# Performance work log

Measured on AMD Instinct MI355X. Metric: run time of the kernel, lower is better.

## Reference

```python
import jax, jax.numpy as jnp
import numpy as np

EPS = 1e-5
CURVE_LEN = 16


def gather_neighbors(feature, idx):
    # feature: [B, C, N], idx: [B, N, k] -> [B, C, N, k]
    return jax.vmap(lambda f, i: f[:, i])(feature, idx)


def cloud_walk(feature, knn_idx):
    # feature: [B, C, N], knn_idx: [B, N, k] -> walk_index [B, N, 16] (int)
    B, C, N = feature.shape
    neigh = gather_neighbors(feature, knn_idx)                 # [B, C, N, k]
    sim = jnp.einsum('bcn,bcnk->bnk', feature, neigh)          # [B, N, k]
    attn = jax.nn.softmax(sim, axis=-1)
    top4 = jax.lax.top_k(attn, 4)[1]                           # [B, N, 4]
    tmp = top4.reshape(B * N, 4)
    nxt = top4[:, :, 1]                                        # [B, N]
    walks = [nxt]
    for _ in range(CURVE_LEN - 1):
        # faithful to original: index rows of tmp by previous step's values
        nxt = tmp[nxt.reshape(-1), 1].reshape(B, N)
        walks.append(nxt)
    return jnp.stack(walks, axis=-1)                           # [B, N, 16]


def self_attention_layer(feature, walk_idx, Wq, bq, Wk, bk, Wv, bv, gamma, beta):
    # feature: [B, C, N], walk_idx: [B, N, 16]
    wf = gather_neighbors(feature, walk_idx)                   # [B, C, N, 16]
    wf = jnp.transpose(wf, (0, 2, 3, 1))                       # [B, N, 16, C]
    center = jnp.transpose(feature, (0, 2, 1))[:, :, None, :]  # [B, N, 1, C]
    win = jnp.concatenate([wf, center], axis=2)                # [B, N, 17, C]
    Q = win @ Wq.T + bq
    K = win @ Wk.T + bk
    V = win @ Wv.T + bv
    sim = jnp.einsum('bnic,bnjc->bnij', Q, K)                  # [B, N, 17, 17]
    attn = jax.nn.softmax(sim, axis=-1)
    # original einsum 'bnkk,bnkc->bnc' => diagonal of attention weights V
    d = jnp.diagonal(attn, axis1=2, axis2=3)                   # [B, N, 17]
    out = jnp.einsum('bnk,bnkc->bnc', d, V)                    # [B, N, C]
    x = jnp.transpose(out, (0, 2, 1))                          # [B, C, N]
    # BatchNorm1d, training mode: stats over (batch, points), biased variance
    mean = jnp.mean(x, axis=(0, 2), keepdims=True)
    var = jnp.mean((x - mean) ** 2, axis=(0, 2), keepdims=True)
    x = gamma[None, :, None] * (x - mean) / jnp.sqrt(var + EPS) + beta[None, :, None]
    x = jax.nn.relu(x)
    return feature + x


def setup_inputs() -> dict:
    key = jax.random.key(0)
    B, C, N, k = 2, 64, 32768, 16
    ks = jax.random.split(key, 10)
    feature = jax.random.normal(ks[0], (B, C, N), dtype=jnp.float32)
    knn_idx = jax.random.randint(ks[1], (B, N, k), 0, N)
    Wq = jax.random.normal(ks[2], (3, C, C), dtype=jnp.float32) * 0.05
    bq = jax.random.normal(ks[3], (3, C), dtype=jnp.float32) * 0.05
    Wk = jax.random.normal(ks[4], (3, C, C), dtype=jnp.float32) * 0.05
    bk = jax.random.normal(ks[5], (3, C), dtype=jnp.float32) * 0.05
    Wv = jax.random.normal(ks[6], (3, C, C), dtype=jnp.float32) * 0.05
    bv = jax.random.normal(ks[7], (3, C), dtype=jnp.float32) * 0.05
    gamma = jnp.ones((3, C), dtype=jnp.float32)
    beta = jnp.zeros((3, C), dtype=jnp.float32)
    return {"feature": feature, "knn_idx": knn_idx, "Wq": Wq, "bq": bq,
            "Wk": Wk, "bk": bk, "Wv": Wv, "bv": bv, "gamma": gamma, "beta": beta}


def reference(feature, knn_idx, Wq, bq, Wk, bk, Wv, bv, gamma, beta):
    walk_idx = cloud_walk(feature, knn_idx)
    heads = []
    f = feature
    for i in range(3):
        f = self_attention_layer(f, walk_idx, Wq[i], bq[i], Wk[i], bk[i],
                                 Wv[i], bv[i], gamma[i], beta[i])
        heads.append(f)
    return jnp.concatenate(heads, axis=1)  # [B, 3C, N]
```

## Files before the change

### kernel.cpp

```cpp
#include <hip/hip_runtime.h>
#include <math.h>

#define NB 2
#define NC 64
#define NN 32768
#define NPTS (NB*NN)
#define NWAVES 1056
#define NSLOTS 67584

typedef _Float16 half_t;
typedef _Float16 f16x8 __attribute__((ext_vector_type(8)));
typedef _Float16 f16x4 __attribute__((ext_vector_type(4)));
typedef float f32x4 __attribute__((ext_vector_type(4)));

__global__ void k_transpose(const float* __restrict__ f, float* __restrict__ fT,
                            half_t* __restrict__ xh) {
    int blk = blockIdx.x;
    int b = blk / (NN/64);
    int n0 = (blk % (NN/64)) * 64;
    __shared__ float tile[64][65];
    int t = threadIdx.x;
    int dn = t & 63, c0 = t >> 6;
    for (int i = 0; i < 16; ++i) {
        int c = c0 + i*4;
        tile[c][dn] = f[((size_t)(b*NC + c))*NN + n0 + dn];
    }
    __syncthreads();
    int o = t & 63, d0 = t >> 6;
    for (int i = 0; i < 16; ++i) {
        int dn2 = d0 + i*4;
        size_t idx = ((size_t)(b*NN + n0 + dn2))*64 + o;
        float v = tile[o][dn2];
        fT[idx] = v;
        xh[idx] = (half_t)v;
    }
}

__global__ __launch_bounds__(256, 4) void k_s2(const float* __restrict__ fT,
                                               const int* __restrict__ knn,
                                               int* __restrict__ s2buf) {
    int t = threadIdx.x;
    int gp = blockIdx.x * 32 + (t >> 3);
    int l8 = t & 7;
    int q4 = l8 & 3;
    int h  = l8 >> 2;
    int b = gp >> 15;
    const float4* cen4 = (const float4*)(fT + (size_t)gp*64 + q4*16);
    float4 c0 = cen4[0], c1 = cen4[1], c2 = cen4[2], c3 = cen4[3];
    float own[8];
    #pragma unroll
    for (int kk = 0; kk < 8; ++kk) {
        int idx = knn[(gp << 4) + h*8 + kk];
        const float4* nb = (const float4*)(fT + ((size_t)(b*NN + idx))*64 + q4*16);
        float4 n0 = nb[0], n1 = nb[1], n2 = nb[2], n3 = nb[3];
        double a = 0.0;
        a += (double)c0.x*(double)n0.x + (double)c0.y*(double)n0.y
           + (double)c0.z*(double)n0.z + (double)c0.w*(double)n0.w;
        a += (double)c1.x*(double)n1.x + (double)c1.y*(double)n1.y
           + (double)c1.z*(double)n1.z + (double)c1.w*(double)n1.w;
        a += (double)c2.x*(double)n2.x + (double)c2.y*(double)n2.y
           + (double)c2.z*(double)n2.z + (double)c2.w*(double)n2.w;
        a += (double)c3.x*(double)n3.x + (double)c3.y*(double)n3.y
           + (double)c3.z*(double)n3.z + (double)c3.w*(double)n3.w;
        a += __shfl_xor(a, 1, 64);
        a += __shfl_xor(a, 2, 64);
        own[kk] = (float)a;
    }
    float sims[16];
    #pragma unroll
    for (int kk = 0; kk < 8; ++kk) {
        float oth = __shfl_xor(own[kk], 4, 64);
        sims[kk]     = h ? oth : own[kk];
        sims[kk + 8] = h ? own[kk] : oth;
    }
    float m = sims[0];
    #pragma unroll
    for (int k = 1; k < 16; ++k) m = fmaxf(m, sims[k]);
    float e[16]; float Z = 0.f;
    #pragma unroll
    for (int k = 0; k < 16; ++k) { e[k] = expf(sims[k]-m); Z += e[k]; }
    float b1 = -1.f, b2 = -1.f; int i1 = -1, i2 = -1;
    #pragma unroll
    for (int k = 0; k < 16; ++k) {
        float a = e[k]/Z;
        if (a > b1)      { b2 = b1; i2 = i1; b1 = a; i1 = k; }
        else if (a > b2) { b2 = a; i2 = k; }
    }
    if (l8 == 0) s2buf[gp] = i2;
}

__global__ void k_walk(const int* __restrict__ s2buf, int* __restrict__ walkrows) {
    __shared__ int T[16];
    int t = threadIdx.x;
    if (t < 16) T[t] = s2buf[t];
    __syncthreads();
    if (t < 16) {
        int w = t;
        walkrows[t*16 + 0] = w;
        for (int s = 1; s < 16; ++s) { w = T[w]; walkrows[t*16 + s] = w; }
    }
}

__global__ void k_init(int* __restrict__ slotlist, int* __restrict__ wavebucket) {
    int idx = blockIdx.x*256 + threadIdx.x;
    if (idx < NSLOTS) slotlist[idx] = -1;
    if (idx < NWAVES) wavebucket[idx] = -1;
}

__global__ void k_hist2(const int* __restrict__ s2buf, int* __restrict__ bh) {
    __shared__ int hst[32];
    int t = threadIdx.x, blk = blockIdx.x;
    if (t < 32) hst[t] = 0;
    __syncthreads();
    int p = blk*256 + t;
    int bucket = (p >> 15)*16 + s2buf[p];
    atomicAdd(&hst[bucket], 1);
    __syncthreads();
    if (t < 32) bh[t*256 + blk] = hst[t];
}

__global__ void k_prefix(const int* __restrict__ bh, int* __restrict__ blockoff,
                         int* __restrict__ wavebucket) {
    __shared__ int tot[32], wst[32];
    int t = threadIdx.x;
    if (t < 32) {
        int s = 0;
        for (int b = 0; b < 256; ++b) s += bh[t*256 + b];
        tot[t] = s;
    }
    __syncthreads();
    if (t == 0) {
        int off = 0;
        for (int i = 0; i < 32; ++i) {
            wst[i] = off;
            off += ((tot[i] + 63) >> 6) << 6;
        }
    }
    __syncthreads();
    if (t < 32) {
        int run = wst[t];
        for (int b = 0; b < 256; ++b) {
            blockoff[t*256 + b] = run;
            run += bh[t*256 + b];
        }
        int w0 = wst[t] >> 6, nw = (tot[t] + 63) >> 6;
        for (int w = 0; w < nw; ++w) wavebucket[w0 + w] = t;
    }
}

__global__ void k_scatter2(const int* __restrict__ s2buf,
                           const int* __restrict__ blockoff,
                           int* __restrict__ slotlist) {
    __shared__ int hst[32], base[32];
    int t = threadIdx.x, blk = blockIdx.x;
    if (t < 32) { hst[t] = 0; base[t] = blockoff[t*256 + blk]; }
    __syncthreads();
    int p = blk*256 + t;
    int bucket = (p >> 15)*16 + s2buf[p];
    int r = atomicAdd(&hst[bucket], 1);
    slotlist[base[bucket] + r] = p;
}

__global__ __launch_bounds__(256) void k_precomp(
        const float* __restrict__ fT,
        const float* __restrict__ Wq, const float* __restrict__ bq,
        const float* __restrict__ Wk, const float* __restrict__ bk,
        const float* __restrict__ Wv, const float* __restrict__ bv,
        const int* __restrict__ walkrows,
        half_t* __restrict__ Pq16, half_t* __restrict__ Pk16,
        half_t* __restrict__ PvT16, float* __restrict__ Pstat,
        half_t* __restrict__ wh) {
    int blk = blockIdx.x;
    int b = blk >> 4, sv = blk & 15;
    size_t bsv16 = (size_t)(b*16 + sv) * 1024;
    int bs48 = (b*16 + sv)*48;
    __shared__ float win[16][64];
    __shared__ float Wl[64][65];
    __shared__ float qw[16][65], kw[16][65];
    __shared__ float simw[16][17];
    __shared__ int wr[16];
    int t = threadIdx.x;
    #pragma unroll
    for (int j = 0; j < 2; ++j) {
        int idx = j*8192 + blk*256 + t;
        if (idx < 12288) {
            float v = idx < 4096 ? Wq[idx] : (idx < 8192 ? Wk[idx-4096] : Wv[idx-8192]);
            wh[idx] = (half_t)v;
        }
    }
    if (t < 16) wr[t] = walkrows[sv*16 + t];
    __syncthreads();
    #pragma unroll
    for (int i = 0; i < 4; ++i) {
        int idx = t + i*256; int tt = idx >> 6, c = idx & 63;
        win[tt][c] = fT[((size_t)(b*NN + wr[tt]))*64 + c];
    }
    int wv = t >> 6, lane = t & 63;
    for (int m = 0; m < 3; ++m) {
        const float* W  = m == 0 ? Wq : (m == 1 ? Wk : Wv);
        const float* bb = m == 0 ? bq : (m == 1 ? bk : bv);
        __syncthreads();
        #pragma unroll
        for (int i = 0; i < 16; ++i) {
            int idx = t + i*256;
            Wl[idx >> 6][idx & 63] = W[idx];
        }
        __syncthreads();
        float acc[4] = {0.f, 0.f, 0.f, 0.f};
        for (int c = 0; c < 64; ++c) {
            float w_ = Wl[lane][c];
            #pragma unroll
            for (int r = 0; r < 4; ++r) acc[r] = fmaf(w_, win[wv*4 + r][c], acc[r]);
        }
        float bias = bb[lane];
        #pragma unroll
        for (int r = 0; r < 4; ++r) {
            int tt = wv*4 + r;
            float val = acc[r] + bias;
            if (m == 0)      { qw[tt][lane] = val; Pq16[bsv16 + tt*64 + lane] = (half_t)val; }
            else if (m == 1) { kw[tt][lane] = val; Pk16[bsv16 + tt*64 + lane] = (half_t)val; }
            else             {                     PvT16[bsv16 + lane*16 + tt] = (half_t)val; }
        }
    }
    __syncthreads();
    {
        int i = t >> 4, j = t & 15;
        float acc = 0.f;
        for (int o = 0; o < 64; ++o) acc = fmaf(qw[i][o], kw[j][o], acc);
        simw[i][j] = acc;
    }
    __syncthreads();
    if (t < 16) {
        float mx = simw[t][0];
        for (int j = 1; j < 16; ++j) mx = fmaxf(mx, simw[t][j]);
        float z = 0.f;
        for (int j = 0; j < 16; ++j) z += expf(simw[t][j] - mx);
        Pstat[bs48 + t*3 + 0] = mx;
        Pstat[bs48 + t*3 + 1] = z;
        Pstat[bs48 + t*3 + 2] = simw[t][t];
    }
}

__global__ __launch_bounds__(256) void k_gemm(
        const half_t* __restrict__ xh, const int* __restrict__ slotlist, int s0,
        const half_t* __restrict__ wh,
        const float* __restrict__ bq, const float* __restrict__ bk,
        const float* __restrict__ bv,
        half_t* __restrict__ qh, half_t* __restrict__ kh, half_t* __restrict__ vh) {
    __shared__ __align__(16) half_t XO[256*72];
    __shared__ __align__(16) half_t WL[192*72];
    int t = threadIdx.x;
    int lane = t & 63, wv = t >> 6;
    size_t go = (size_t)blockIdx.x * 256 * 64;
    {
        int srow = slotlist[s0 + blockIdx.x*256 + t];
        int prow = srow < 0 ? 0 : srow;
        const uint4* src = (const uint4*)(xh + (size_t)prow*64);
        #pragma unroll
        for (int j = 0; j < 8; ++j) *(uint4*)&XO[t*72 + j*8] = src[j];
    }
    #pragma unroll
    for (int j = 0; j < 6; ++j) {
        int idx8 = t + j*256;
        int row = idx8 >> 3, c0 = (idx8 & 7) * 8;
        *(uint4*)&WL[row*72 + c0] = *(const uint4*)(wh + idx8*8);
    }
    __syncthreads();
    int m15 = lane & 15, k0 = (lane >> 4) * 8;
    int ar = wv*64 + m15;
    f16x8 a00 = *(const f16x8*)&XO[(ar    )*72 + k0];
    f16x8 a01 = *(const f16x8*)&XO[(ar    )*72 + k0 + 32];
    f16x8 a10 = *(const f16x8*)&XO[(ar+16)*72 + k0];
    f16x8 a11 = *(const f16x8*)&XO[(ar+16)*72 + k0 + 32];
    f16x8 a20 = *(const f16x8*)&XO[(ar+32)*72 + k0];
    f16x8 a21 = *(const f16x8*)&XO[(ar+32)*72 + k0 + 32];
    f16x8 a30 = *(const f16x8*)&XO[(ar+48)*72 + k0];
    f16x8 a31 = *(const f16x8*)&XO[(ar+48)*72 + k0 + 32];
    __syncthreads();
    #pragma unroll 1
    for (int m = 0; m < 3; ++m) {
        const float* bias = m == 0 ? bq : (m == 1 ? bk : bv);
        half_t* outp      = m == 0 ? qh : (m == 1 ? kh : vh);
        int wb = m*64 + m15;
        f16x8 b00 = *(const f16x8*)&WL[(wb    )*72 + k0];
        f16x8 b01 = *(const f16x8*)&WL[(wb    )*72 + k0 + 32];
        f16x8 b10 = *(const f16x8*)&WL[(wb+16)*72 + k0];
        f16x8 b11 = *(const f16x8*)&WL[(wb+16)*72 + k0 + 32];
        f16x8 b20 = *(const f16x8*)&WL[(wb+32)*72 + k0];
        f16x8 b21 = *(const f16x8*)&WL[(wb+32)*72 + k0 + 32];
        f16x8 b30 = *(const f16x8*)&WL[(wb+48)*72 + k0];
        f16x8 b31 = *(const f16x8*)&WL[(wb+48)*72 + k0 + 32];
        float bs0 = bias[m15], bs1 = bias[16+m15], bs2 = bias[32+m15], bs3 = bias[48+m15];
        f32x4 Z = {0.f, 0.f, 0.f, 0.f};
        f32x4 c00=Z,c01=Z,c02=Z,c03=Z, c10=Z,c11=Z,c12=Z,c13=Z;
        f32x4 c20=Z,c21=Z,c22=Z,c23=Z, c30=Z,c31=Z,c32=Z,c33=Z;
        #define MM(i,j) \
            c##i##j = __builtin_amdgcn_mfma_f32_16x16x32_f16(a##i##0, b##j##0, c##i##j, 0,0,0); \
            c##i##j = __builtin_amdgcn_mfma_f32_16x16x32_f16(a##i##1, b##j##1, c##i##j, 0,0,0);
        MM(0,0) MM(0,1) MM(0,2) MM(0,3)
        MM(1,0) MM(1,1) MM(1,2) MM(1,3)
        MM(2,0) MM(2,1) MM(2,2) MM(2,3)
        MM(3,0) MM(3,1) MM(3,2) MM(3,3)
        #undef MM
        __syncthreads();
        int r0 = wv*64 + ((lane >> 4) << 2);
        #define WR(i,j,bsj) { \
            XO[(r0 + i*16 + 0)*64 + j*16 + m15] = (half_t)(c##i##j[0] + bsj); \
            XO[(r0 + i*16 + 1)*64 + j*16 + m15] = (half_t)(c##i##j[1] + bsj); \
            XO[(r0 + i*16 + 2)*64 + j*16 + m15] = (half_t)(c##i##j[2] + bsj); \
            XO[(r0 + i*16 + 3)*64 + j*16 + m15] = (half_t)(c##i##j[3] + bsj); }
        WR(0,0,bs0) WR(0,1,bs1) WR(0,2,bs2) WR(0,3,bs3)
        WR(1,0,bs0) WR(1,1,bs1) WR(1,2,bs2) WR(1,3,bs3)
        WR(2,0,bs0) WR(2,1,bs1) WR(2,2,bs2) WR(2,3,bs3)
        WR(3,0,bs0) WR(3,1,bs1) WR(3,2,bs2) WR(3,3,bs3)
        #undef WR
        __syncthreads();
        #pragma unroll
        for (int j = 0; j < 8; ++j) {
            int idx = (j*256 + t) * 8;
            *(uint4*)(outp + go + idx) = *(const uint4*)&XO[idx];
        }
    }
}

__global__ __launch_bounds__(256) void k_comb4(
        const half_t* __restrict__ qh, const half_t* __restrict__ kh,
        const half_t* __restrict__ vh,
        const half_t* __restrict__ Pq16, const half_t* __restrict__ Pk16,
        const half_t* __restrict__ PvT16, const float* __restrict__ Pstat,
        const int* __restrict__ slotlist, const int* __restrict__ wavebucket,
        half_t* __restrict__ xo, int s0) {
    int t = threadIdx.x, j = t >> 6, lane = t & 63;
    int wslot = blockIdx.x*64;
    int gbase = s0 + wslot;
    int bucket = wavebucket[gbase >> 6];
    if (bucket < 0) return;
    int m15 = lane & 15, g4 = lane >> 4;
    int k0h = g4 * 8;
    size_t bsv16 = (size_t)bucket << 10;
    int bs48 = bucket * 48;

    f16x8 pqA0 = *(const f16x8*)&Pq16[bsv16 + m15*64 + k0h];
    f16x8 pqA1 = *(const f16x8*)&Pq16[bsv16 + m15*64 + k0h + 32];
    f16x8 pkA0 = *(const f16x8*)&Pk16[bsv16 + m15*64 + k0h];
    f16x8 pkA1 = *(const f16x8*)&Pk16[bsv16 + m15*64 + k0h + 32];
    f16x4 pvB0 = *(const f16x4*)&PvT16[bsv16 + (0*16 + m15)*16 + g4*4];
    f16x4 pvB1 = *(const f16x4*)&PvT16[bsv16 + (1*16 + m15)*16 + g4*4];
    f16x4 pvB2 = *(const f16x4*)&PvT16[bsv16 + (2*16 + m15)*16 + g4*4];
    f16x4 pvB3 = *(const f16x4*)&PvT16[bsv16 + (3*16 + m15)*16 + g4*4];
    float pm[4], pz[4], dg[4];
    #pragma unroll
    for (int r = 0; r < 4; ++r) {
        pm[r] = Pstat[bs48 + (g4*4+r)*3 + 0];
        pz[r] = Pstat[bs48 + (g4*4+r)*3 + 1];
        dg[r] = Pstat[bs48 + (g4*4+r)*3 + 2];
    }
    int4 pid4 = *(const int4*)&slotlist[gbase + j*16 + g4*4];

    const half_t* kp = kh + (size_t)(wslot + j*16 + m15)*64;
    const half_t* qp = qh + (size_t)(wslot + j*16 + m15)*64;
    f16x8 kB0 = *(const f16x8*)&kp[k0h];
    f16x8 kB1 = *(const f16x8*)&kp[k0h + 32];
    f16x8 qB0 = *(const f16x8*)&qp[k0h];
    f16x8 qB1 = *(const f16x8*)&qp[k0h + 32];
    f32x4 Zz = {0.f,0.f,0.f,0.f};
    f32x4 sp = __builtin_amdgcn_mfma_f32_16x16x32_f16(pqA0, kB0, Zz, 0,0,0);
    sp = __builtin_amdgcn_mfma_f32_16x16x32_f16(pqA1, kB1, sp, 0,0,0);
    f32x4 tp = __builtin_amdgcn_mfma_f32_16x16x32_f16(pkA0, qB0, Zz, 0,0,0);
    tp = __builtin_amdgcn_mfma_f32_16x16x32_f16(pkA1, qB1, tp, 0,0,0);
    float up = 0.f;
    #pragma unroll
    for (int e = 0; e < 8; ++e) {
        up = fmaf((float)qB0[e], (float)kB0[e], up);
        up = fmaf((float)qB1[e], (float)kB1[e], up);
    }
    up += __shfl_xor(up, 16, 64);
    up += __shfl_xor(up, 32, 64);
    float d0, d1, d2, d3;
    {
        float mi, zi;
        mi = fmaxf(pm[0], sp[0]); zi = pz[0]*expf(pm[0]-mi) + expf(sp[0]-mi); d0 = expf(dg[0]-mi)/zi;
        mi = fmaxf(pm[1], sp[1]); zi = pz[1]*expf(pm[1]-mi) + expf(sp[1]-mi); d1 = expf(dg[1]-mi)/zi;
        mi = fmaxf(pm[2], sp[2]); zi = pz[2]*expf(pm[2]-mi) + expf(sp[2]-mi); d2 = expf(dg[2]-mi)/zi;
        mi = fmaxf(pm[3], sp[3]); zi = pz[3]*expf(pm[3]-mi) + expf(sp[3]-mi); d3 = expf(dg[3]-mi)/zi;
    }
    float tmax = fmaxf(fmaxf(tp[0], tp[1]), fmaxf(tp[2], tp[3]));
    tmax = fmaxf(tmax, __shfl_xor(tmax, 16, 64));
    tmax = fmaxf(tmax, __shfl_xor(tmax, 32, 64));
    float mc = fmaxf(tmax, up);
    float ze = expf(tp[0]-mc) + expf(tp[1]-mc) + expf(tp[2]-mc) + expf(tp[3]-mc);
    ze += __shfl_xor(ze, 16, 64);
    ze += __shfl_xor(ze, 32, 64);
    float ec = expf(up - mc);
    float dcen = ec / (ze + ec);
    f16x4 dA; dA[0] = (half_t)d0; dA[1] = (half_t)d1; dA[2] = (half_t)d2; dA[3] = (half_t)d3;

    float dc0 = __shfl(dcen, g4*4 + 0, 64);
    float dc1 = __shfl(dcen, g4*4 + 1, 64);
    float dc2 = __shfl(dcen, g4*4 + 2, 64);
    float dc3 = __shfl(dcen, g4*4 + 3, 64);
    int p0 = pid4.x, p1 = pid4.y, p2 = pid4.z, p3 = pid4.w;
    size_t vb0 = (size_t)(wslot + j*16 + g4*4 + 0)*64;
    size_t vb1 = (size_t)(wslot + j*16 + g4*4 + 1)*64;
    size_t vb2 = (size_t)(wslot + j*16 + g4*4 + 2)*64;
    size_t vb3 = (size_t)(wslot + j*16 + g4*4 + 3)*64;
    #pragma unroll
    for (int jc = 0; jc < 4; ++jc) {
        f16x4 pvB = jc == 0 ? pvB0 : (jc == 1 ? pvB1 : (jc == 2 ? pvB2 : pvB3));
        f32x4 Z2 = {0.f,0.f,0.f,0.f};
        f32x4 acc = __builtin_amdgcn_mfma_f32_16x16x16f16(dA, pvB, Z2, 0,0,0);
        int c = jc*16 + m15;
        float v0 = (float)vh[vb0 + c];
        float v1 = (float)vh[vb1 + c];
        float v2 = (float)vh[vb2 + c];
        float v3 = (float)vh[vb3 + c];
        if (p0 >= 0) xo[(size_t)p0*64 + c] = (half_t)(acc[0] + dc0*v0);
        if (p1 >= 0) xo[(size_t)p1*64 + c] = (half_t)(acc[1] + dc1*v1);
        if (p2 >= 0) xo[(size_t)p2*64 + c] = (half_t)(acc[2] + dc2*v2);
        if (p3 >= 0) xo[(size_t)p3*64 + c] = (half_t)(acc[3] + dc3*v3);
    }
}

__global__ __launch_bounds__(256) void k_reduce(const half_t* __restrict__ x,
                                                float* __restrict__ part) {
    __shared__ float ls[4][64], lq[4][64];
    int t = threadIdx.x, q = t >> 6, c = t & 63;
    size_t base = ((size_t)blockIdx.x*128 + q*32) * 64;
    float s = 0.f, sq = 0.f;
    for (int r = 0; r < 32; ++r) {
        float v = (float)x[base + r*64 + c];
        s += v; sq = fmaf(v, v, sq);
    }
    ls[q][c] = s; lq[q][c] = sq;
    __syncthreads();
    if (q == 0) {
        float S = ls[0][c] + ls[1][c] + ls[2][c] + ls[3][c];
        float Q = lq[0][c] + lq[1][c] + lq[2][c] + lq[3][c];
        part[blockIdx.x*64 + c] = S;
        part[512*64 + blockIdx.x*64 + c] = Q;
    }
}

__global__ __launch_bounds__(256) void k_stats(const float* __restrict__ part,
                                               float* __restrict__ mv) {
    __shared__ float ls[4][64], lq[4][64];
    int t = threadIdx.x, q = t >> 6, c = t & 63;
    float s = 0.f, sq = 0.f;
    for (int r = q*128; r < q*128 + 128; ++r) {
        s  += part[r*64 + c];
        sq += part[512*64 + r*64 + c];
    }
    ls[q][c] = s; lq[q][c] = sq;
    __syncthreads();
    if (q == 0) {
        float S = ls[0][c] + ls[1][c] + ls[2][c] + ls[3][c];
        float Q = lq[0][c] + lq[1][c] + lq[2][c] + lq[3][c];
        float mean = S / (float)NPTS;
        float var  = Q / (float)NPTS - mean*mean;
        mv[c] = mean; mv[64 + c] = var;
    }
}

__global__ void k_norm(const half_t* __restrict__ x, float* __restrict__ fT,
                       const float* __restrict__ mv,
                       const float* __restrict__ gamma, const float* __restrict__ beta,
                       float* __restrict__ out, int l, half_t* __restrict__ xh) {
    int blk = blockIdx.x;
    int b = blk / (NN/64);
    int n0 = (blk % (NN/64)) * 64;
    __shared__ float tile[64][65];
    int t = threadIdx.x;
    int c = t & 63, d0 = t >> 6;
    float mean = mv[c], var = mv[64+c];
    float inv = 1.0f / sqrtf(var + 1e-5f);
    float ga = gamma[c], be = beta[c];
    for (int i = 0; i < 16; ++i) {
        int dn = d0 + i*4;
        size_t pi = ((size_t)(b*NN + n0 + dn))*64 + c;
        float xv = (float)x[pi];
        float y = fT[pi] + fmaxf(ga * (xv - mean) * inv + be, 0.f);
        fT[pi] = y;
        xh[pi] = (half_t)y;
        tile[dn][c] = y;
    }
    __syncthreads();
    int dn2 = t & 63, c0 = t >> 6;
    for (int i = 0; i < 16; ++i) {
        int cc = c0 + i*4;
        out[((size_t)(b*192 + l*64 + cc))*NN + n0 + dn2] = tile[dn2][cc];
    }
}

extern "C" void kernel_launch(void* const* d_in, const int* in_sizes, int n_in,
                              void* d_out, int out_size, void* d_ws, size_t ws_size,
                              hipStream_t stream) {
    const float* feature = (const float*)d_in[0];
    const int*   knn     = (const int*)d_in[1];
    const float* Wq = (const float*)d_in[2];
    const float* bq = (const float*)d_in[3];
    const float* Wk = (const float*)d_in[4];
    const float* bk = (const float*)d_in[5];
    const float* Wv = (const float*)d_in[6];
    const float* bv = (const float*)d_in[7];
    const float* gamma = (const float*)d_in[8];
    const float* beta  = (const float*)d_in[9];
    float* out = (float*)d_out;

    char* ws = (char*)d_ws;
    float*  fT    = (float*) ws;
    half_t* xh    = (half_t*)(ws + 16777216);
    half_t* xo    = (half_t*)(ws + 25165824);
    int*    s2buf = (int*)   (ws + 33554432);
    int*    walkrows = (int*)(ws + 33816576);
    half_t* Pq16  = (half_t*)(ws + 33817600);
    half_t* Pk16  = (half_t*)(ws + 33883136);
    half_t* PvT16 = (half_t*)(ws + 33948672);
    float*  Pstat = (float*) (ws + 34014208);
    float*  part  = (float*) (ws + 34020352);
    float*  mv    = (float*) (ws + 34282496);
    half_t* wh    = (half_t*)(ws + 34283008);
    int*    bh        = (int*)(ws + 34307584);
    int*    blockoff  = (int*)(ws + 34340352);
    int*    wavebucket= (int*)(ws + 34373120);
    int*    slotlist  = (int*)(ws + 34377344);
    size_t  qkv_off = 34647680;

    size_t avail = ws_size > qkv_off ? ws_size - qkv_off : 0;
    size_t chunk = avail / 384;
    chunk = (chunk / 256) * 256;
    if (chunk > (size_t)NSLOTS) chunk = NSLOTS;
    if (chunk < 256) chunk = 256;
    half_t* qh = (half_t*)(ws + qkv_off);
    half_t* kh = qh + chunk*64;
    half_t* vh = kh + chunk*64;

    k_transpose<<<NB*(NN/64), 256, 0, stream>>>(feature, fT, xh);
    k_s2<<<NPTS/32, 256, 0, stream>>>(fT, knn, s2buf);
    k_walk<<<1, 64, 0, stream>>>(s2buf, walkrows);
    k_init<<<NSLOTS/256, 256, 0, stream>>>(slotlist, wavebucket);
    k_hist2<<<NPTS/256, 256, 0, stream>>>(s2buf, bh);
    k_prefix<<<1, 256, 0, stream>>>(bh, blockoff, wavebucket);
    k_scatter2<<<NPTS/256, 256, 0, stream>>>(s2buf, blockoff, slotlist);

    for (int l = 0; l < 3; ++l) {
        k_precomp<<<32, 256, 0, stream>>>(fT, Wq + l*4096, bq + l*64,
                                          Wk + l*4096, bk + l*64,
                                          Wv + l*4096, bv + l*64,
                                          walkrows, Pq16, Pk16, PvT16, Pstat, wh);
        for (size_t s0 = 0; s0 < NSLOTS; s0 += chunk) {
            size_t cn = (s0 + chunk <= NSLOTS) ? chunk : (NSLOTS - s0);
            k_gemm<<<(unsigned)(cn/256), 256, 0, stream>>>(xh, slotlist, (int)s0, wh,
                                                           bq + l*64, bk + l*64, bv + l*64,
                                                           qh, kh, vh);
            k_comb4<<<(unsigned)(cn/64), 256, 0, stream>>>(qh, kh, vh,
                                                           Pq16, Pk16, PvT16, Pstat,
                                                           slotlist, wavebucket,
                                                           xo, (int)s0);
        }
        k_reduce<<<512, 256, 0, stream>>>(xo, part);
        k_stats<<<1, 256, 0, stream>>>(part, mv);
        k_norm<<<NB*(NN/64), 256, 0, stream>>>(xo, fT, mv, gamma + l*64, beta + l*64,
                                               out, l, xh);
    }
}
```

Before: 221.8 us.

## Fuse QKV GEMM with attention combine and merge setup kernels

The per-layer QKV projection and the attention-combine step now run in one kernel. Q, K and V stay in LDS instead of being written to and re-read from global memory, and the chunked launch loop goes away. The walk and slotlist/wavebucket initialisation are folded into k_prefix, which removes two launches. In exchange, blocks are smaller (128 threads), weights are read straight from global memory instead of staged in LDS, and the padding-slot init now runs in a single block.

```diff
diff --git a/kernel.cpp b/kernel.cpp
--- a/kernel.cpp
+++ b/kernel.cpp
@@ -89,52 +89,43 @@
     if (l8 == 0) s2buf[gp] = i2;
 }
 
-__global__ void k_walk(const int* __restrict__ s2buf, int* __restrict__ walkrows) {
+__global__ void k_hist2(const int* __restrict__ s2buf, int* __restrict__ bh) {
+    __shared__ int hst[32];
+    int t = threadIdx.x, blk = blockIdx.x;
+    if (t < 32) hst[t] = 0;
+    __syncthreads();
+    int p = blk*256 + t;
+    int bucket = (p >> 15)*16 + s2buf[p];
+    atomicAdd(&hst[bucket], 1);
+    __syncthreads();
+    if (t < 32) bh[t*256 + blk] = hst[t];
+}
+
+__global__ void k_prefix(const int* __restrict__ s2buf, const int* __restrict__ bh,
+                         int* __restrict__ blockoff, int* __restrict__ wavebucket,
+                         int* __restrict__ slotlist, int* __restrict__ walkrows) {
+    __shared__ int tot[32], wst[32], offsh;
     __shared__ int T[16];
     int t = threadIdx.x;
     if (t < 16) T[t] = s2buf[t];
+    if (t < 32) {
+        int s = 0;
+        for (int b = 0; b < 256; ++b) s += bh[t*256 + b];
+        tot[t] = s;
+    }
     __syncthreads();
     if (t < 16) {
         int w = t;
         walkrows[t*16 + 0] = w;
         for (int s = 1; s < 16; ++s) { w = T[w]; walkrows[t*16 + s] = w; }
     }
-}
-
-__global__ void k_init(int* __restrict__ slotlist, int* __restrict__ wavebucket) {
-    int idx = blockIdx.x*256 + threadIdx.x;
-    if (idx < NSLOTS) slotlist[idx] = -1;
-    if (idx < NWAVES) wavebucket[idx] = -1;
-}
-
-__global__ void k_hist2(const int* __restrict__ s2buf, int* __restrict__ bh) {
-    __shared__ int hst[32];
-    int t = threadIdx.x, blk = blockIdx.x;
-    if (t < 32) hst[t] = 0;
-    __syncthreads();
-    int p = blk*256 + t;
-    int bucket = (p >> 15)*16 + s2buf[p];
-    atomicAdd(&hst[bucket], 1);
-    __syncthreads();
-    if (t < 32) bh[t*256 + blk] = hst[t];
-}
-
-__global__ void k_prefix(const int* __restrict__ bh, int* __restrict__ blockoff,
-                         int* __restrict__ wavebucket) {
-    __shared__ int tot[32], wst[32];
-    int t = threadIdx.x;
-    if (t < 32) {
-        int s = 0;
-        for (int b = 0; b < 256; ++b) s += bh[t*256 + b];
-        tot[t] = s;
-    }
-    __syncthreads();
     if (t == 0) {
         int off = 0;
         for (int i = 0; i < 32; ++i) {
             wst[i] = off;
             off += ((tot[i] + 63) >> 6) << 6;
         }
+        offsh = off;
     }
     __syncthreads();
     if (t < 32) {
@@ -145,7 +136,12 @@
         }
         int w0 = wst[t] >> 6, nw = (tot[t] + 63) >> 6;
         for (int w = 0; w < nw; ++w) wavebucket[w0 + w] = t;
-    }
+        for (int s = wst[t] + tot[t]; s < wst[t] + nw*64; ++s) slotlist[s] = -1;
+    }
+    __syncthreads();
+    int off = offsh;
+    for (int w = (off >> 6) + t; w < NWAVES; w += 256) wavebucket[w] = -1;
+    for (int s = off + t; s < NSLOTS; s += 256) slotlist[s] = -1;
 }
 
 __global__ void k_scatter2(const int* __restrict__ s2buf,
@@ -241,55 +237,53 @@
     }
 }
 
-__global__ __launch_bounds__(256) void k_gemm(
-        const half_t* __restrict__ xh, const int* __restrict__ slotlist, int s0,
-        const half_t* __restrict__ wh,
+__global__ __launch_bounds__(128) void k_fused(
+        const half_t* __restrict__ xh, const int* __restrict__ slotlist,
+        const int* __restrict__ wavebucket, const half_t* __restrict__ wh,
         const float* __restrict__ bq, const float* __restrict__ bk,
         const float* __restrict__ bv,
-        half_t* __restrict__ qh, half_t* __restrict__ kh, half_t* __restrict__ vh) {
-    __shared__ __align__(16) half_t XO[256*72];
-    __shared__ __align__(16) half_t WL[192*72];
+        const half_t* __restrict__ Pq16, const half_t* __restrict__ Pk16,
+        const half_t* __restrict__ PvT16, const float* __restrict__ Pstat,
+        half_t* __restrict__ xo) {
+    __shared__ __align__(16) half_t Qs[128*72];
+    __shared__ __align__(16) half_t Ks[128*72];
+    __shared__ __align__(16) half_t Vs[128*72];
     int t = threadIdx.x;
     int lane = t & 63, wv = t >> 6;
-    size_t go = (size_t)blockIdx.x * 256 * 64;
+    int base = blockIdx.x * 128;
     {
-        int srow = slotlist[s0 + blockIdx.x*256 + t];
+        int srow = slotlist[base + t];
         int prow = srow < 0 ? 0 : srow;
         const uint4* src = (const uint4*)(xh + (size_t)prow*64);
         #pragma unroll
-        for (int j = 0; j < 8; ++j) *(uint4*)&XO[t*72 + j*8] = src[j];
-    }
-    #pragma unroll
-    for (int j = 0; j < 6; ++j) {
-        int idx8 = t + j*256;
-        int row = idx8 >> 3, c0 = (idx8 & 7) * 8;
-        *(uint4*)&WL[row*72 + c0] = *(const uint4*)(wh + idx8*8);
-    }
-    __syncthreads();
-    int m15 = lane & 15, k0 = (lane >> 4) * 8;
+        for (int j = 0; j < 8; ++j) *(uint4*)&Qs[t*72 + j*8] = src[j];
+    }
+    __syncthreads();
+    int m15 = lane & 15, g4 = lane >> 4;
+    int k0 = g4 * 8;
     int ar = wv*64 + m15;
-    f16x8 a00 = *(const f16x8*)&XO[(ar    )*72 + k0];
-    f16x8 a01 = *(const f16x8*)&XO[(ar    )*72 + k0 + 32];
-    f16x8 a10 = *(const f16x8*)&XO[(ar+16)*72 + k0];
-    f16x8 a11 = *(const f16x8*)&XO[(ar+16)*72 + k0 + 32];
-    f16x8 a20 = *(const f16x8*)&XO[(ar+32)*72 + k0];
-    f16x8 a21 = *(const f16x8*)&XO[(ar+32)*72 + k0 + 32];
-    f16x8 a30 = *(const f16x8*)&XO[(ar+48)*72 + k0];
-    f16x8 a31 = *(const f16x8*)&XO[(ar+48)*72 + k0 + 32];
+    f16x8 a00 = *(const f16x8*)&Qs[(ar    )*72 + k0];
+    f16x8 a01 = *(const f16x8*)&Qs[(ar    )*72 + k0 + 32];
+    f16x8 a10 = *(const f16x8*)&Qs[(ar+16)*72 + k0];
+    f16x8 a11 = *(const f16x8*)&Qs[(ar+16)*72 + k0 + 32];
+    f16x8 a20 = *(const f16x8*)&Qs[(ar+32)*72 + k0];
+    f16x8 a21 = *(const f16x8*)&Qs[(ar+32)*72 + k0 + 32];
+    f16x8 a30 = *(const f16x8*)&Qs[(ar+48)*72 + k0];
+    f16x8 a31 = *(const f16x8*)&Qs[(ar+48)*72 + k0 + 32];
     __syncthreads();
     #pragma unroll 1
     for (int m = 0; m < 3; ++m) {
         const float* bias = m == 0 ? bq : (m == 1 ? bk : bv);
-        half_t* outp      = m == 0 ? qh : (m == 1 ? kh : vh);
-        int wb = m*64 + m15;
-        f16x8 b00 = *(const f16x8*)&WL[(wb    )*72 + k0];
-        f16x8 b01 = *(const f16x8*)&WL[(wb    )*72 + k0 + 32];
-        f16x8 b10 = *(const f16x8*)&WL[(wb+16)*72 + k0];
-        f16x8 b11 = *(const f16x8*)&WL[(wb+16)*72 + k0 + 32];
-        f16x8 b20 = *(const f16x8*)&WL[(wb+32)*72 + k0];
-        f16x8 b21 = *(const f16x8*)&WL[(wb+32)*72 + k0 + 32];
-        f16x8 b30 = *(const f16x8*)&WL[(wb+48)*72 + k0];
-        f16x8 b31 = *(const f16x8*)&WL[(wb+48)*72 + k0 + 32];
+        half_t* outL      = m == 0 ? Qs : (m == 1 ? Ks : Vs);
+        const half_t* wrow = wh + m*4096;
+        f16x8 b00 = *(const f16x8*)&wrow[(m15   )*64 + k0];
+        f16x8 b01 = *(const f16x8*)&wrow[(m15   )*64 + k0 + 32];
+        f16x8 b10 = *(const f16x8*)&wrow[(m15+16)*64 + k0];
+        f16x8 b11 = *(const f16x8*)&wrow[(m15+16)*64 + k0 + 32];
+        f16x8 b20 = *(const f16x8*)&wrow[(m15+32)*64 + k0];
+        f16x8 b21 = *(const f16x8*)&wrow[(m15+32)*64 + k0 + 32];
+        f16x8 b30 = *(const f16x8*)&wrow[(m15+48)*64 + k0];
+        f16x8 b31 = *(const f16x8*)&wrow[(m15+48)*64 + k0 + 32];
         float bs0 = bias[m15], bs1 = bias[16+m15], bs2 = bias[32+m15], bs3 = bias[48+m15];
         f32x4 Z = {0.f, 0.f, 0.f, 0.f};
         f32x4 c00=Z,c01=Z,c02=Z,c03=Z, c10=Z,c11=Z,c12=Z,c13=Z;
@@ -302,48 +296,28 @@
         MM(2,0) MM(2,1) MM(2,2) MM(2,3)
         MM(3,0) MM(3,1) MM(3,2) MM(3,3)
         #undef MM
-        __syncthreads();
-        int r0 = wv*64 + ((lane >> 4) << 2);
+        int r0 = wv*64 + g4*4;
         #define WR(i,j,bsj) { \
-            XO[(r0 + i*16 + 0)*64 + j*16 + m15] = (half_t)(c##i##j[0] + bsj); \
-            XO[(r0 + i*16 + 1)*64 + j*16 + m15] = (half_t)(c##i##j[1] + bsj); \
-            XO[(r0 + i*16 + 2)*64 + j*16 + m15] = (half_t)(c##i##j[2] + bsj); \
-            XO[(r0 + i*16 + 3)*64 + j*16 + m15] = (half_t)(c##i##j[3] + bsj); }
+            outL[(r0 + i*16 + 0)*72 + j*16 + m15] = (half_t)(c##i##j[0] + bsj); \
+            outL[(r0 + i*16 + 1)*72 + j*16 + m15] = (half_t)(c##i##j[1] + bsj); \
+            outL[(r0 + i*16 + 2)*72 + j*16 + m15] = (half_t)(c##i##j[2] + bsj); \
+            outL[(r0 + i*16 + 3)*72 + j*16 + m15] = (half_t)(c##i##j[3] + bsj); }
         WR(0,0,bs0) WR(0,1,bs1) WR(0,2,bs2) WR(0,3,bs3)
         WR(1,0,bs0) WR(1,1,bs1) WR(1,2,bs2) WR(1,3,bs3)
         WR(2,0,bs0) WR(2,1,bs1) WR(2,2,bs2) WR(2,3,bs3)
         WR(3,0,bs0) WR(3,1,bs1) WR(3,2,bs2) WR(3,3,bs3)
         #undef WR
-        __syncthreads();
-        #pragma unroll
-        for (int j = 0; j < 8; ++j) {
-            int idx = (j*256 + t) * 8;
-            *(uint4*)(outp + go + idx) = *(const uint4*)&XO[idx];
-        }
-    }
-}
-
-__global__ __launch_bounds__(256) void k_comb4(
-        const half_t* __restrict__ qh, const half_t* __restrict__ kh,
-        const half_t* __restrict__ vh,
-        const half_t* __restrict__ Pq16, const half_t* __restrict__ Pk16,
-        const half_t* __restrict__ PvT16, const float* __restrict__ Pstat,
-        const int* __restrict__ slotlist, const int* __restrict__ wavebucket,
-        half_t* __restrict__ xo, int s0) {
-    int t = threadIdx.x, j = t >> 6, lane = t & 63;
-    int wslot = blockIdx.x*64;
-    int gbase = s0 + wslot;
-    int bucket = wavebucket[gbase >> 6];
+    }
+    __syncthreads();
+    int gslot = base + wv*64;
+    int bucket = wavebucket[gslot >> 6];
     if (bucket < 0) return;
-    int m15 = lane & 15, g4 = lane >> 4;
-    int k0h = g4 * 8;
     size_t bsv16 = (size_t)bucket << 10;
     int bs48 = bucket * 48;
-
-    f16x8 pqA0 = *(const f16x8*)&Pq16[bsv16 + m15*64 + k0h];
-    f16x8 pqA1 = *(const f16x8*)&Pq16[bsv16 + m15*64 + k0h + 32];
-    f16x8 pkA0 = *(const f16x8*)&Pk16[bsv16 + m15*64 + k0h];
-    f16x8 pkA1 = *(const f16x8*)&Pk16[bsv16 + m15*64 + k0h + 32];
+    f16x8 pqA0 = *(const f16x8*)&Pq16[bsv16 + m15*64 + k0];
+    f16x8 pqA1 = *(const f16x8*)&Pq16[bsv16 + m15*64 + k0 + 32];
+    f16x8 pkA0 = *(const f16x8*)&Pk16[bsv16 + m15*64 + k0];
+    f16x8 pkA1 = *(const f16x8*)&Pk16[bsv16 + m15*64 + k0 + 32];
     f16x4 pvB0 = *(const f16x4*)&PvT16[bsv16 + (0*16 + m15)*16 + g4*4];
     f16x4 pvB1 = *(const f16x4*)&PvT16[bsv16 + (1*16 + m15)*16 + g4*4];
     f16x4 pvB2 = *(const f16x4*)&PvT16[bsv16 + (2*16 + m15)*16 + g4*4];
@@ -355,69 +329,67 @@
         pz[r] = Pstat[bs48 + (g4*4+r)*3 + 1];
         dg[r] = Pstat[bs48 + (g4*4+r)*3 + 2];
     }
-    int4 pid4 = *(const int4*)&slotlist[gbase + j*16 + g4*4];
-
-    const half_t* kp = kh + (size_t)(wslot + j*16 + m15)*64;
-    const half_t* qp = qh + (size_t)(wslot + j*16 + m15)*64;
-    f16x8 kB0 = *(const f16x8*)&kp[k0h];
-    f16x8 kB1 = *(const f16x8*)&kp[k0h + 32];
-    f16x8 qB0 = *(const f16x8*)&qp[k0h];
-    f16x8 qB1 = *(const f16x8*)&qp[k0h + 32];
-    f32x4 Zz = {0.f,0.f,0.f,0.f};
-    f32x4 sp = __builtin_amdgcn_mfma_f32_16x16x32_f16(pqA0, kB0, Zz, 0,0,0);
-    sp = __builtin_amdgcn_mfma_f32_16x16x32_f16(pqA1, kB1, sp, 0,0,0);
-    f32x4 tp = __builtin_amdgcn_mfma_f32_16x16x32_f16(pkA0, qB0, Zz, 0,0,0);
-    tp = __builtin_amdgcn_mfma_f32_16x16x32_f16(pkA1, qB1, tp, 0,0,0);
-    float up = 0.f;
-    #pragma unroll
-    for (int e = 0; e < 8; ++e) {
-        up = fmaf((float)qB0[e], (float)kB0[e], up);
-        up = fmaf((float)qB1[e], (float)kB1[e], up);
-    }
-    up += __shfl_xor(up, 16, 64);
-    up += __shfl_xor(up, 32, 64);
-    float d0, d1, d2, d3;
-    {
-        float mi, zi;
-        mi = fmaxf(pm[0], sp[0]); zi = pz[0]*expf(pm[0]-mi) + expf(sp[0]-mi); d0 = expf(dg[0]-mi)/zi;
-        mi = fmaxf(pm[1], sp[1]); zi = pz[1]*expf(pm[1]-mi) + expf(sp[1]-mi); d1 = expf(dg[1]-mi)/zi;
-        mi = fmaxf(pm[2], sp[2]); zi = pz[2]*expf(pm[2]-mi) + expf(sp[2]-mi); d2 = expf(dg[2]-mi)/zi;
-        mi = fmaxf(pm[3], sp[3]); zi = pz[3]*expf(pm[3]-mi) + expf(sp[3]-mi); d3 = expf(dg[3]-mi)/zi;
-    }
-    float tmax = fmaxf(fmaxf(tp[0], tp[1]), fmaxf(tp[2], tp[3]));
-    tmax = fmaxf(tmax, __shfl_xor(tmax, 16, 64));
-    tmax = fmaxf(tmax, __shfl_xor(tmax, 32, 64));
-    float mc = fmaxf(tmax, up);
-    float ze = expf(tp[0]-mc) + expf(tp[1]-mc) + expf(tp[2]-mc) + expf(tp[3]-mc);
-    ze += __shfl_xor(ze, 16, 64);
-    ze += __shfl_xor(ze, 32, 64);
-    float ec = expf(up - mc);
-    float dcen = ec / (ze + ec);
-    f16x4 dA; dA[0] = (half_t)d0; dA[1] = (half_t)d1; dA[2] = (half_t)d2; dA[3] = (half_t)d3;
-
-    float dc0 = __shfl(dcen, g4*4 + 0, 64);
-    float dc1 = __shfl(dcen, g4*4 + 1, 64);
-    float dc2 = __shfl(dcen, g4*4 + 2, 64);
-    float dc3 = __shfl(dcen, g4*4 + 3, 64);
-    int p0 = pid4.x, p1 = pid4.y, p2 = pid4.z, p3 = pid4.w;
-    size_t vb0 = (size_t)(wslot + j*16 + g4*4 + 0)*64;
-    size_t vb1 = (size_t)(wslot + j*16 + g4*4 + 1)*64;
-    size_t vb2 = (size_t)(wslot + j*16 + g4*4 + 2)*64;
-    size_t vb3 = (size_t)(wslot + j*16 + g4*4 + 3)*64;
-    #pragma unroll
-    for (int jc = 0; jc < 4; ++jc) {
-        f16x4 pvB = jc == 0 ? pvB0 : (jc == 1 ? pvB1 : (jc == 2 ? pvB2 : pvB3));
-        f32x4 Z2 = {0.f,0.f,0.f,0.f};
-        f32x4 acc = __builtin_amdgcn_mfma_f32_16x16x16f16(dA, pvB, Z2, 0,0,0);
-        int c = jc*16 + m15;
-        float v0 = (float)vh[vb0 + c];
-        float v1 = (float)vh[vb1 + c];
-        float v2 = (float)vh[vb2 + c];
-        float v3 = (float)vh[vb3 + c];
-        if (p0 >= 0) xo[(size_t)p0*64 + c] = (half_t)(acc[0] + dc0*v0);
-        if (p1 >= 0) xo[(size_t)p1*64 + c] = (half_t)(acc[1] + dc1*v1);
-        if (p2 >= 0) xo[(size_t)p2*64 + c] = (half_t)(acc[2] + dc2*v2);
-        if (p3 >= 0) xo[(size_t)p3*64 + c] = (half_t)(acc[3] + dc3*v3);
+    #pragma unroll 1
+    for (int j = 0; j < 4; ++j) {
+        int lrow = wv*64 + j*16 + m15;
+        const half_t* kp = &Ks[lrow*72];
+        const half_t* qp = &Qs[lrow*72];
+        f16x8 kB0 = *(const f16x8*)&kp[k0];
+        f16x8 kB1 = *(const f16x8*)&kp[k0 + 32];
+        f16x8 qB0 = *(const f16x8*)&qp[k0];
+        f16x8 qB1 = *(const f16x8*)&qp[k0 + 32];
+        f32x4 Zz = {0.f,0.f,0.f,0.f};
+        f32x4 sp = __builtin_amdgcn_mfma_f32_16x16x32_f16(pqA0, kB0, Zz, 0,0,0);
+        sp = __builtin_amdgcn_mfma_f32_16x16x32_f16(pqA1, kB1, sp, 0,0,0);
+        f32x4 tp = __builtin_amdgcn_mfma_f32_16x16x32_f16(pkA0, qB0, Zz, 0,0,0);
+        tp = __builtin_amdgcn_mfma_f32_16x16x32_f16(pkA1, qB1, tp, 0,0,0);
+        float up = 0.f;
+        #pragma unroll
+        for (int e = 0; e < 8; ++e) {
+            up = fmaf((float)qB0[e], (float)kB0[e], up);
+            up = fmaf((float)qB1[e], (float)kB1[e], up);
+        }
+        up += __shfl_xor(up, 16, 64);
+        up += __shfl_xor(up, 32, 64);
+        float d0, d1, d2, d3;
+        {
+            float mi, zi;
+            mi = fmaxf(pm[0], sp[0]); zi = pz[0]*expf(pm[0]-mi) + expf(sp[0]-mi); d0 = expf(dg[0]-mi)/zi;
+            mi = fmaxf(pm[1], sp[1]); zi = pz[1]*expf(pm[1]-mi) + expf(sp[1]-mi); d1 = expf(dg[1]-mi)/zi;
+            mi = fmaxf(pm[2], sp[2]); zi = pz[2]*expf(pm[2]-mi) + expf(sp[2]-mi); d2 = expf(dg[2]-mi)/zi;
+            mi = fmaxf(pm[3], sp[3]); zi = pz[3]*expf(pm[3]-mi) + expf(sp[3]-mi); d3 = expf(dg[3]-mi)/zi;
+        }
+        float tmax = fmaxf(fmaxf(tp[0], tp[1]), fmaxf(tp[2], tp[3]));
+        tmax = fmaxf(tmax, __shfl_xor(tmax, 16, 64));
+        tmax = fmaxf(tmax, __shfl_xor(tmax, 32, 64));
+        float mc = fmaxf(tmax, up);
+        float ze = expf(tp[0]-mc) + expf(tp[1]-mc) + expf(tp[2]-mc) + expf(tp[3]-mc);
+        ze += __shfl_xor(ze, 16, 64);
+        ze += __shfl_xor(ze, 32, 64);
+        float ec = expf(up - mc);
+        float dcen = ec / (ze + ec);
+        f16x4 dA; dA[0] = (half_t)d0; dA[1] = (half_t)d1; dA[2] = (half_t)d2; dA[3] = (half_t)d3;
+        float dc0 = __shfl(dcen, g4*4 + 0, 64);
+        float dc1 = __shfl(dcen, g4*4 + 1, 64);
+        float dc2 = __shfl(dcen, g4*4 + 2, 64);
+        float dc3 = __shfl(dcen, g4*4 + 3, 64);
+        int4 pid4 = *(const int4*)&slotlist[gslot + j*16 + g4*4];
+        int vr0 = wv*64 + j*16 + g4*4;
+        #pragma unroll
+        for (int jc = 0; jc < 4; ++jc) {
+            f16x4 pvB = jc == 0 ? pvB0 : (jc == 1 ? pvB1 : (jc == 2 ? pvB2 : pvB3));
+            f32x4 Z2 = {0.f,0.f,0.f,0.f};
+            f32x4 acc = __builtin_amdgcn_mfma_f32_16x16x16f16(dA, pvB, Z2, 0,0,0);
+            int c = jc*16 + m15;
+            float v0 = (float)Vs[(vr0+0)*72 + c];
+            float v1 = (float)Vs[(vr0+1)*72 + c];
+            float v2 = (float)Vs[(vr0+2)*72 + c];
+            float v3 = (float)Vs[(vr0+3)*72 + c];
+            if (pid4.x >= 0) xo[(size_t)pid4.x*64 + c] = (half_t)(acc[0] + dc0*v0);
+            if (pid4.y >= 0) xo[(size_t)pid4.y*64 + c] = (half_t)(acc[1] + dc1*v1);
+            if (pid4.z >= 0) xo[(size_t)pid4.z*64 + c] = (half_t)(acc[2] + dc2*v2);
+            if (pid4.w >= 0) xo[(size_t)pid4.w*64 + c] = (half_t)(acc[3] + dc3*v3);
+        }
     }
 }
 
@@ -523,23 +495,11 @@
     int*    blockoff  = (int*)(ws + 34340352);
     int*    wavebucket= (int*)(ws + 34373120);
     int*    slotlist  = (int*)(ws + 34377344);
-    size_t  qkv_off = 34647680;
-
-    size_t avail = ws_size > qkv_off ? ws_size - qkv_off : 0;
-    size_t chunk = avail / 384;
-    chunk = (chunk / 256) * 256;
-    if (chunk > (size_t)NSLOTS) chunk = NSLOTS;
-    if (chunk < 256) chunk = 256;
-    half_t* qh = (half_t*)(ws + qkv_off);
-    half_t* kh = qh + chunk*64;
-    half_t* vh = kh + chunk*64;
 
     k_transpose<<<NB*(NN/64), 256, 0, stream>>>(feature, fT, xh);
     k_s2<<<NPTS/32, 256, 0, stream>>>(fT, knn, s2buf);
-    k_walk<<<1, 64, 0, stream>>>(s2buf, walkrows);
-    k_init<<<NSLOTS/256, 256, 0, stream>>>(slotlist, wavebucket);
     k_hist2<<<NPTS/256, 256, 0, stream>>>(s2buf, bh);
-    k_prefix<<<1, 256, 0, stream>>>(bh, blockoff, wavebucket);
+    k_prefix<<<1, 256, 0, stream>>>(s2buf, bh, blockoff, wavebucket, slotlist, walkrows);
     k_scatter2<<<NPTS/256, 256, 0, stream>>>(s2buf, blockoff, slotlist);
 
     for (int l = 0; l < 3; ++l) {
@@ -547,16 +507,9 @@
                                           Wk + l*4096, bk + l*64,
                                           Wv + l*4096, bv + l*64,
                                           walkrows, Pq16, Pk16, PvT16, Pstat, wh);
-        for (size_t s0 = 0; s0 < NSLOTS; s0 += chunk) {
-            size_t cn = (s0 + chunk <= NSLOTS) ? chunk : (NSLOTS - s0);
-            k_gemm<<<(unsigned)(cn/256), 256, 0, stream>>>(xh, slotlist, (int)s0, wh,
-                                                           bq + l*64, bk + l*64, bv + l*64,
-                                                           qh, kh, vh);
-            k_comb4<<<(unsigned)(cn/64), 256, 0, stream>>>(qh, kh, vh,
-                                                           Pq16, Pk16, PvT16, Pstat,
-                                                           slotlist, wavebucket,
-                                                           xo, (int)s0);
-        }
+        k_fused<<<NSLOTS/128, 128, 0, stream>>>(xh, slotlist, wavebucket, wh,
+                                                bq + l*64, bk + l*64, bv + l*64,
+                                                Pq16, Pk16, PvT16, Pstat, xo);
         k_reduce<<<512, 256, 0, stream>>>(xo, part);
         k_stats<<<1, 256, 0, stream>>>(part, mv);
         k_norm<<<NB*(NN/64), 256, 0, stream>>>(xo, fT, mv, gamma + l*64, beta + l*64,
```

Result: slower. 233.3 us (+5.2%).

## Fold walk and slot-init into prefix kernel; widen k_s2 to 16 lanes per point

Applied to the files above, without the earlier changes.

k_s2 now uses 16 lanes per point instead of 8, each lane handling 4 neighbours rather than 8. The 16 similarities are then gathered with shuffles. This raises parallelism and shortens each lane's serial gather chain, at the cost of twice as many blocks. The separate k_walk and k_init launches are removed. Walk-row building and the -1 padding of slotlist and wavebucket move into the single-block k_prefix kernel, which saves two launches but makes one block write most of the tail padding serially.

```diff
diff --git a/kernel.cpp b/kernel.cpp
--- a/kernel.cpp
+++ b/kernel.cpp
@@ -40,17 +40,17 @@
                                                const int* __restrict__ knn,
                                                int* __restrict__ s2buf) {
     int t = threadIdx.x;
-    int gp = blockIdx.x * 32 + (t >> 3);
-    int l8 = t & 7;
-    int q4 = l8 & 3;
-    int h  = l8 >> 2;
+    int gp = blockIdx.x * 16 + (t >> 4);
+    int l16 = t & 15;
+    int q4 = l16 & 3;
+    int h4 = l16 >> 2;
     int b = gp >> 15;
     const float4* cen4 = (const float4*)(fT + (size_t)gp*64 + q4*16);
     float4 c0 = cen4[0], c1 = cen4[1], c2 = cen4[2], c3 = cen4[3];
-    float own[8];
-    #pragma unroll
-    for (int kk = 0; kk < 8; ++kk) {
-        int idx = knn[(gp << 4) + h*8 + kk];
+    float own[4];
+    #pragma unroll
+    for (int kk = 0; kk < 4; ++kk) {
+        int idx = knn[(gp << 4) + h4*4 + kk];
         const float4* nb = (const float4*)(fT + ((size_t)(b*NN + idx))*64 + q4*16);
         float4 n0 = nb[0], n1 = nb[1], n2 = nb[2], n3 = nb[3];
         double a = 0.0;
@@ -66,13 +66,11 @@
         a += __shfl_xor(a, 2, 64);
         own[kk] = (float)a;
     }
+    int base16 = t & 48;
     float sims[16];
     #pragma unroll
-    for (int kk = 0; kk < 8; ++kk) {
-        float oth = __shfl_xor(own[kk], 4, 64);
-        sims[kk]     = h ? oth : own[kk];
-        sims[kk + 8] = h ? own[kk] : oth;
-    }
+    for (int j = 0; j < 16; ++j)
+        sims[j] = __shfl(own[j & 3], base16 + ((j >> 2) << 2), 64);
     float m = sims[0];
     #pragma unroll
     for (int k = 1; k < 16; ++k) m = fmaxf(m, sims[k]);
@@ -86,55 +84,46 @@
         if (a > b1)      { b2 = b1; i2 = i1; b1 = a; i1 = k; }
         else if (a > b2) { b2 = a; i2 = k; }
     }
-    if (l8 == 0) s2buf[gp] = i2;
-}
-
-__global__ void k_walk(const int* __restrict__ s2buf, int* __restrict__ walkrows) {
+    if (l16 == 0) s2buf[gp] = i2;
+}
+
+__global__ void k_hist2(const int* __restrict__ s2buf, int* __restrict__ bh) {
+    __shared__ int hst[32];
+    int t = threadIdx.x, blk = blockIdx.x;
+    if (t < 32) hst[t] = 0;
+    __syncthreads();
+    int p = blk*256 + t;
+    int bucket = (p >> 15)*16 + s2buf[p];
+    atomicAdd(&hst[bucket], 1);
+    __syncthreads();
+    if (t < 32) bh[t*256 + blk] = hst[t];
+}
+
+__global__ void k_prefix(const int* __restrict__ s2buf, const int* __restrict__ bh,
+                         int* __restrict__ blockoff, int* __restrict__ wavebucket,
+                         int* __restrict__ slotlist, int* __restrict__ walkrows) {
+    __shared__ int tot[32], wst[32], offsh;
     __shared__ int T[16];
     int t = threadIdx.x;
     if (t < 16) T[t] = s2buf[t];
+    if (t < 32) {
+        int s = 0;
+        for (int b = 0; b < 256; ++b) s += bh[t*256 + b];
+        tot[t] = s;
+    }
     __syncthreads();
     if (t < 16) {
         int w = t;
         walkrows[t*16 + 0] = w;
         for (int s = 1; s < 16; ++s) { w = T[w]; walkrows[t*16 + s] = w; }
     }
-}
-
-__global__ void k_init(int* __restrict__ slotlist, int* __restrict__ wavebucket) {
-    int idx = blockIdx.x*256 + threadIdx.x;
-    if (idx < NSLOTS) slotlist[idx] = -1;
-    if (idx < NWAVES) wavebucket[idx] = -1;
-}
-
-__global__ void k_hist2(const int* __restrict__ s2buf, int* __restrict__ bh) {
-    __shared__ int hst[32];
-    int t = threadIdx.x, blk = blockIdx.x;
-    if (t < 32) hst[t] = 0;
-    __syncthreads();
-    int p = blk*256 + t;
-    int bucket = (p >> 15)*16 + s2buf[p];
-    atomicAdd(&hst[bucket], 1);
-    __syncthreads();
-    if (t < 32) bh[t*256 + blk] = hst[t];
-}
-
-__global__ void k_prefix(const int* __restrict__ bh, int* __restrict__ blockoff,
-                         int* __restrict__ wavebucket) {
-    __shared__ int tot[32], wst[32];
-    int t = threadIdx.x;
-    if (t < 32) {
-        int s = 0;
-        for (int b = 0; b < 256; ++b) s += bh[t*256 + b];
-        tot[t] = s;
-    }
-    __syncthreads();
     if (t == 0) {
         int off = 0;
         for (int i = 0; i < 32; ++i) {
             wst[i] = off;
             off += ((tot[i] + 63) >> 6) << 6;
         }
+        offsh = off;
     }
     __syncthreads();
     if (t < 32) {
@@ -145,7 +134,12 @@
         }
         int w0 = wst[t] >> 6, nw = (tot[t] + 63) >> 6;
         for (int w = 0; w < nw; ++w) wavebucket[w0 + w] = t;
-    }
+        for (int s = wst[t] + tot[t]; s < wst[t] + nw*64; ++s) slotlist[s] = -1;
+    }
+    __syncthreads();
+    int off = offsh;
+    for (int w = (off >> 6) + t; w < NWAVES; w += 256) wavebucket[w] = -1;
+    for (int s = off + t; s < NSLOTS; s += 256) slotlist[s] = -1;
 }
 
 __global__ void k_scatter2(const int* __restrict__ s2buf,
@@ -535,11 +529,9 @@
     half_t* vh = kh + chunk*64;
 
     k_transpose<<<NB*(NN/64), 256, 0, stream>>>(feature, fT, xh);
-    k_s2<<<NPTS/32, 256, 0, stream>>>(fT, knn, s2buf);
-    k_walk<<<1, 64, 0, stream>>>(s2buf, walkrows);
-    k_init<<<NSLOTS/256, 256, 0, stream>>>(slotlist, wavebucket);
+    k_s2<<<NPTS/16, 256, 0, stream>>>(fT, knn, s2buf);
     k_hist2<<<NPTS/256, 256, 0, stream>>>(s2buf, bh);
-    k_prefix<<<1, 256, 0, stream>>>(bh, blockoff, wavebucket);
+    k_prefix<<<1, 256, 0, stream>>>(s2buf, bh, blockoff, wavebucket, slotlist, walkrows);
     k_scatter2<<<NPTS/256, 256, 0, stream>>>(s2buf, blockoff, slotlist);
 
     for (int l = 0; l < 3; ++l) {
```

New measurement: 219.7 us. Within noise of the previous version (-0.9%).
